# Performance work log

Hardware: AMD Instinct MI355X
Metric: run time of the kernel (lower is better)

## Reference

```python
import jax, jax.numpy as jnp
import numpy as np

J, T, N_VARS, K = 64, 64, 4, 8   # n_inputs, terms per input poly, vars, Bernstein coeffs per var
I = 64                            # layer_size (output nodes)


def setup_inputs() -> dict:
    key = jax.random.key(0)
    k1, k2, k3, k4, k5, k6 = jax.random.split(key, 6)
    return {
        "layer_inputs_under": jax.random.normal(k1, (J, T, N_VARS, K), jnp.float32),
        "layer_inputs_over": jax.random.normal(k2, (J, T, N_VARS, K), jnp.float32),
        "layer_inputs_under_degrees": jax.random.randint(k3, (J, N_VARS), 0, 5).astype(jnp.float32),
        "layer_inputs_over_degrees": jax.random.randint(k4, (J, N_VARS), 0, 5).astype(jnp.float32),
        "layer_weights": jax.random.normal(k5, (I, J), jnp.float32),
        "layer_biases": jax.random.normal(k6, (I,), jnp.float32),
    }


def _scale_polys(polys, w):
    """mult_with_constant, vectorized over nodes and inputs.
    In IBF a polynomial is scaled by a constant by scaling the FIRST variable's
    coefficient row of every term.  polys: [J,T,n,k], w: [I,J] -> [I,J,T,n,k]."""
    i = w.shape[0]
    row0 = polys[None, :, :, 0:1, :] * w[:, :, None, None, None]        # [I,J,T,1,k]
    rest = jnp.broadcast_to(polys[None, :, :, 1:, :],
                            (i, polys.shape[0], polys.shape[1], polys.shape[2] - 1, polys.shape[3]))
    return jnp.concatenate([row0, rest], axis=3)


def _layer(liu, lio, w, b):
    """LayerModule.forward with activation='linear' (identity path of NodeModule).
    node_under = sum_j (w_neg[i,j]*over_j + w_pos[i,j]*under_j) + bias term
    node_over  = sum_j (w_pos[i,j]*over_j + w_neg[i,j]*under_j) + bias term
    sum_2_polys == concatenation of term lists; add_with_constant appends one
    constant term (row0 = bias, remaining variable rows = ones)."""
    w_pos = jax.nn.relu(w)
    w_neg = -jax.nn.relu(-w)
    j, t, n, k = liu.shape
    i = w.shape[0]

    def combine(wa, wb):
        pa = _scale_polys(lio, wa).reshape(i, j * t, n, k)  # scaled over-polys
        pb = _scale_polys(liu, wb).reshape(i, j * t, n, k)  # scaled under-polys
        return jnp.concatenate([pa, pb], axis=1)            # [I, 2JT, n, k]

    under = combine(w_neg, w_pos)
    over = combine(w_pos, w_neg)

    bias_term = jnp.concatenate(
        [b[:, None, None, None] * jnp.ones((i, 1, 1, k), b.dtype),
         jnp.ones((i, 1, n - 1, k), b.dtype)], axis=2)      # [I,1,n,k]
    under = jnp.concatenate([under, bias_term], axis=1)     # [I, 2JT+1, n, k]
    over = jnp.concatenate([over, bias_term], axis=1)
    return under, over


def reference(layer_inputs_under, layer_inputs_over, layer_inputs_under_degrees,
              layer_inputs_over_degrees, layer_weights, layer_biases):
    under, over = _layer(layer_inputs_under, layer_inputs_over, layer_weights, layer_biases)
    # degree of each node poly = elementwise max of contributing input degrees
    deg = jnp.maximum(layer_inputs_under_degrees, layer_inputs_over_degrees).max(axis=0)  # [n]
    i = layer_weights.shape[0]
    under_deg = jnp.broadcast_to(deg, (i, deg.shape[0]))
    over_deg = under_deg
    return under, over, under_deg, over_deg
```

## Files before the change

kernel.cpp:

```cpp
#include <hip/hip_runtime.h>

namespace {
constexpr int Jc = 64, Tc = 64, NVc = 4, Ic = 64;
constexpr int F4_TERM  = 8;
constexpr int TERMS    = 2 * Jc * Tc + 1;
constexpr int NODE_F4  = TERMS * F4_TERM;
constexpr int TILE_F4  = Tc * F4_TERM;
constexpr long long SIDE_F4 = (long long)Ic * NODE_F4;
constexpr long long DEG_BASE_FLT = 2LL * SIDE_F4 * 4;
constexpr int IG = 8;
constexpr int MAIN_BLOCKS = 2 * 2 * Jc * (Ic / IG);
}

typedef float v4f __attribute__((ext_vector_type(4)));

__device__ __forceinline__ void store4(float4* p, float x, float y, float z, float w) {
    v4f v = {x, y, z, w};
    *reinterpret_cast<v4f*>(p) = v;
}

__global__ __launch_bounds__(256) void layer_kernel(
    const float4* __restrict__ liu,
    const float4* __restrict__ lio,
    const float*  __restrict__ ud,
    const float*  __restrict__ od,
    const float*  __restrict__ w,
    const float*  __restrict__ bias,
    float*        __restrict__ outf)
{
    float4* out = reinterpret_cast<float4*>(outf);
    const int b   = blockIdx.x;
    const int tid = (int)threadIdx.x;

    if (b < MAIN_BLOCKS) {
        const int ig = b & 7;
        const int jj = (b >> 3) & 127;
        const int s  = b >> 10;
        const int h  = jj >> 6;
        const int j  = jj & 63;
        const int i0 = ig * IG;

        const float4* src = (h ? liu : lio) + j * TILE_F4;
        const float4 va = src[tid];
        const float4 vb = src[tid + 256];
        const bool isv0 = (tid & 7) < 2;

        float sv[IG];
        #pragma unroll
        for (int t = 0; t < IG; ++t) {
            const float wv = w[(i0 + t) * Jc + j];
            const float wp = fmaxf(wv, 0.0f);
            const float wn = fminf(wv, 0.0f);
            sv[t] = (h == s) ? wn : wp;
        }

        float4* dst = out + (long long)s * SIDE_F4 + (long long)i0 * NODE_F4
                          + (long long)jj * TILE_F4 + tid;
        #pragma unroll
        for (int t = 0; t < IG; ++t) {
            const float sc = isv0 ? sv[t] : 1.0f;
            store4(dst,       va.x * sc, va.y * sc, va.z * sc, va.w * sc);
            store4(dst + 256, vb.x * sc, vb.y * sc, vb.z * sc, vb.w * sc);
            dst += NODE_F4;
        }
    } else {
        #pragma unroll
        for (int r = 0; r < 4; ++r) {
            const int t    = r * 256 + tid;
            const int reg  = t >> 3;
            const int i    = reg >> 1;
            const int s    = reg & 1;
            const int sub  = t & 7;
            const float val = (sub < 2) ? bias[i] : 1.0f;
            const long long off = (long long)s * SIDE_F4 + (long long)i * NODE_F4
                                  + (long long)(2 * Jc * Tc) * F4_TERM + sub;
            store4(out + off, val, val, val, val);
        }
        const int lane = tid & 63;
        float m[NVc];
        #pragma unroll
        for (int v = 0; v < NVc; ++v)
            m[v] = fmaxf(ud[lane * NVc + v], od[lane * NVc + v]);
        #pragma unroll
        for (int mask = 1; mask < 64; mask <<= 1) {
            #pragma unroll
            for (int v = 0; v < NVc; ++v)
                m[v] = fmaxf(m[v], __shfl_xor(m[v], mask, 64));
        }
        const float dv = m[tid & 3];
        outf[DEG_BASE_FLT + tid] = dv;
        outf[DEG_BASE_FLT + 256 + tid] = dv;
    }
}

extern "C" void kernel_launch(void* const* d_in, const int* in_sizes, int n_in,
                              void* d_out, int out_size, void* d_ws, size_t ws_size,
                              hipStream_t stream) {
    const float4* liu  = (const float4*)d_in[0];
    const float4* lio  = (const float4*)d_in[1];
    const float*  ud   = (const float*)d_in[2];
    const float*  od   = (const float*)d_in[3];
    const float*  w    = (const float*)d_in[4];
    const float*  bias = (const float*)d_in[5];
    float* outf = (float*)d_out;

    layer_kernel<<<dim3(MAIN_BLOCKS + 1), dim3(256), 0, stream>>>(
        liu, lio, ud, od, w, bias, outf);
}
```

Baseline: 143.2 us.

## Give each block a contiguous output span per node instead of input reuse

Blocks now own a contiguous 64KB span of one output node's term list (8 input tiles) instead of one input tile broadcast to 8 output nodes. Writes become fully contiguous per block and reads come from L2, not reused registers. The intent is better write locality and DRAM page behavior for this store-bound kernel, at the cost of 8x more input reads, which are mostly served from cache.

```diff
diff --git a/kernel.cpp b/kernel.cpp
--- a/kernel.cpp
+++ b/kernel.cpp
@@ -8,8 +8,9 @@
 constexpr int TILE_F4  = Tc * F4_TERM;
 constexpr long long SIDE_F4 = (long long)Ic * NODE_F4;
 constexpr long long DEG_BASE_FLT = 2LL * SIDE_F4 * 4;
-constexpr int IG = 8;
-constexpr int MAIN_BLOCKS = 2 * 2 * Jc * (Ic / IG);
+constexpr int SPANS   = 16;
+constexpr int SPAN_F4 = (2 * Tc * Jc / SPANS) * F4_TERM;
+constexpr int MAIN_BLOCKS = 2 * Ic * SPANS;
 }
 
 typedef float v4f __attribute__((ext_vector_type(4)));
@@ -33,35 +34,35 @@
     const int tid = (int)threadIdx.x;
 
     if (b < MAIN_BLOCKS) {
-        const int ig = b & 7;
-        const int jj = (b >> 3) & 127;
-        const int s  = b >> 10;
-        const int h  = jj >> 6;
-        const int j  = jj & 63;
-        const int i0 = ig * IG;
+        const int p = b & (SPANS - 1);
+        const int i = (b >> 4) & 63;
+        const int s = b >> 10;
 
-        const float4* src = (h ? liu : lio) + j * TILE_F4;
-        const float4 va = src[tid];
-        const float4 vb = src[tid + 256];
+        float sv[8];
+        const float4* srcs[8];
+        #pragma unroll
+        for (int ts = 0; ts < 8; ++ts) {
+            const int jj = p * 8 + ts;
+            const int h  = jj >> 6;
+            const int j  = jj & 63;
+            const float wv = w[i * Jc + j];
+            const float wp = fmaxf(wv, 0.0f);
+            const float wn = fminf(wv, 0.0f);
+            sv[ts]   = (h == s) ? wn : wp;
+            srcs[ts] = (h ? liu : lio) + j * TILE_F4;
+        }
+
         const bool isv0 = (tid & 7) < 2;
 
-        float sv[IG];
+        float4* dst = out + (long long)s * SIDE_F4 + (long long)i * NODE_F4
+                          + p * SPAN_F4;
         #pragma unroll
-        for (int t = 0; t < IG; ++t) {
-            const float wv = w[(i0 + t) * Jc + j];
-            const float wp = fmaxf(wv, 0.0f);
-            const float wn = fminf(wv, 0.0f);
-            sv[t] = (h == s) ? wn : wp;
-        }
-
-        float4* dst = out + (long long)s * SIDE_F4 + (long long)i0 * NODE_F4
-                          + (long long)jj * TILE_F4 + tid;
-        #pragma unroll
-        for (int t = 0; t < IG; ++t) {
-            const float sc = isv0 ? sv[t] : 1.0f;
-            store4(dst,       va.x * sc, va.y * sc, va.z * sc, va.w * sc);
-            store4(dst + 256, vb.x * sc, vb.y * sc, vb.z * sc, vb.w * sc);
-            dst += NODE_F4;
+        for (int r = 0; r < 16; ++r) {
+            const int f  = r * 256 + tid;
+            const int ts = r >> 1;
+            const float4 v = srcs[ts][f & 511];
+            const float sc = isv0 ? sv[ts] : 1.0f;
+            store4(dst + f, v.x * sc, v.y * sc, v.z * sc, v.w * sc);
         }
     } else {
         #pragma unroll
```

Result: no change. 144.4 us (+0.8%).
